# Performance work log

Measured on AMD Instinct MI355X. Metric: run time of the kernel, lower is better.

## Reference

```python
import jax, jax.numpy as jnp
import numpy as np

B, N, D = 1, 4096, 512
H, DH, M, WIN = 8, 64, 4, 512
QK_SCALE = 10.0  # qk_norm_scale


def _l2norm(t):
    # F.normalize(p=2, dim=-1) with groups=1
    n = jnp.linalg.norm(t, axis=-1, keepdims=True)
    return t / jnp.maximum(n, 1e-12)


def _rotate_half(t):
    t1, t2 = jnp.split(t, 2, axis=-1)
    return jnp.concatenate([-t2, t1], axis=-1)


def setup_inputs() -> dict:
    key = jax.random.key(0)
    ks = jax.random.split(key, 9)
    s = 0.02
    x = jax.random.normal(ks[0], (B, N, D), jnp.float32)
    Wq = jax.random.normal(ks[1], (D, H * DH), jnp.float32) * s
    Wk = jax.random.normal(ks[2], (D, H * DH), jnp.float32) * s
    Wv = jax.random.normal(ks[3], (D, H * DH), jnp.float32) * s
    Wg = jax.random.normal(ks[4], (D, H * DH), jnp.float32) * s
    bg = jnp.ones((H * DH,), jnp.float32)  # torch init: bias=1
    Wo = jax.random.normal(ks[5], (H * DH, D), jnp.float32) * s
    mem_k = jax.random.normal(ks[6], (H, M, DH), jnp.float32)
    mem_v = jax.random.normal(ks[7], (H, M, DH), jnp.float32)
    # standard rotary table, duplicated halves so rotate_half pairing matches
    half = DH // 2
    inv = 1.0 / (10000.0 ** (np.arange(half, dtype=np.float32) / half))
    f = np.outer(np.arange(N, dtype=np.float32), inv)  # [N, DH/2]
    freqs = jnp.asarray(np.concatenate([f, f], axis=-1), jnp.float32)  # [N, DH]
    return {"x": x, "Wq": Wq, "Wk": Wk, "Wv": Wv, "Wg": Wg, "bg": bg,
            "Wo": Wo, "mem_k": mem_k, "mem_v": mem_v, "freqs": freqs}


def reference(x, Wq, Wk, Wv, Wg, bg, Wo, mem_k, mem_v, freqs):
    # projections -> b h n d
    def split_heads(t):
        return t.reshape(B, N, H, DH).transpose(0, 2, 1, 3)
    q = split_heads(x @ Wq)
    k = split_heads(x @ Wk)
    v = split_heads(x @ Wv)
    # qk-norm (groups=1), scale handled via QK_SCALE later
    q = _l2norm(q)
    k = _l2norm(k)
    # rotary (l == DH so full head dim is rotated)
    cos = jnp.cos(freqs)  # [N, DH]
    sin = jnp.sin(freqs)
    q = q * cos + _rotate_half(q) * sin
    k = k * cos + _rotate_half(k) * sin
    # memory KV concat (mem_k goes through l2norm under qk_norm)
    mk = jnp.broadcast_to(_l2norm(mem_k)[None], (B, H, M, DH))
    mv = jnp.broadcast_to(mem_v[None], (B, H, M, DH))
    k = jnp.concatenate([mk, k], axis=2)  # [B,H,M+N,DH]
    v = jnp.concatenate([mv, v], axis=2)
    J = N + M
    # local window mask: queries at positions M..J-1, keys at 0..J-1
    rq = jnp.arange(M, J)
    rk = jnp.arange(J)
    dist = rq[:, None] - rk[None, :]
    allowed = (dist <= WIN) & (dist >= -WIN)  # [N, J]
    sim = jnp.einsum('bhid,bhjd->bhij', q, k) * QK_SCALE
    neg = -jnp.finfo(sim.dtype).max
    sim = jnp.where(allowed[None, None], sim, neg)
    attn = jax.nn.softmax(sim, axis=-1)
    out = jnp.einsum('bhij,bhjd->bhid', attn, v)  # [B,H,N,DH]
    out = out.transpose(0, 2, 1, 3).reshape(B, N, H * DH)
    # value gating
    gates = x @ Wg + bg
    out = out * jax.nn.sigmoid(gates)
    return out @ Wo
```

## Files before the change

### kernel.cpp

```cpp
#include <hip/hip_runtime.h>
#include <math.h>

#define TN 4096
#define DM 512
#define NH 8
#define DHD 64
#define MEM 4
#define WINR 512
#define JTOT (TN + MEM)
#define JPAD 4168
#define QK_SCALE 10.0f
#define LDA 40

typedef __attribute__((ext_vector_type(8))) short bf16x8;
typedef __attribute__((ext_vector_type(4))) float f32x4;

__device__ __forceinline__ unsigned short f2bf(float f) {
    unsigned u = __float_as_uint(f);
    u = (u + 0x7FFFu + ((u >> 16) & 1u)) >> 16;
    return (unsigned short)u;
}

__global__ __launch_bounds__(256)
void prep(const float* __restrict__ X, unsigned short* __restrict__ Xb,
          const float* __restrict__ W0, const float* __restrict__ W1,
          const float* __restrict__ W2, const float* __restrict__ W3,
          const float* __restrict__ W4, unsigned short* __restrict__ T,
          const float* __restrict__ freqs, float2* __restrict__ tab,
          const float* __restrict__ mem_k, const float* __restrict__ mem_v,
          unsigned short* __restrict__ k_b, unsigned short* __restrict__ v_b)
{
    const int b = blockIdx.x;
    const int t = threadIdx.x;

    if (b < 2048) {
        int idx = b * 256 + t;
        float4 v = *(const float4*)&X[(size_t)idx * 4];
        *(ushort4*)&Xb[(size_t)idx * 4] =
            make_ushort4(f2bf(v.x), f2bf(v.y), f2bf(v.z), f2bf(v.w));
    } else if (b < 2368) {
        __shared__ unsigned short Ts[64][68];
        int bi = b - 2048;
        int sel = bi >> 6, tile = bi & 63;
        const float* __restrict__ W =
            (sel == 0) ? W0 : (sel == 1) ? W1 : (sel == 2) ? W2 : (sel == 3) ? W3 : W4;
        unsigned short* __restrict__ Wt = T + (size_t)sel * DM * DM;
        int r0 = (tile >> 3) * 64, c0 = (tile & 7) * 64;
        #pragma unroll
        for (int p = 0; p < 4; ++p) {
            int i  = p * 16 + (t >> 4);
            int j4 = (t & 15) * 4;
            float4 v = *(const float4*)&W[(size_t)(r0 + i) * DM + c0 + j4];
            Ts[i][j4 + 0] = f2bf(v.x); Ts[i][j4 + 1] = f2bf(v.y);
            Ts[i][j4 + 2] = f2bf(v.z); Ts[i][j4 + 3] = f2bf(v.w);
        }
        __syncthreads();
        #pragma unroll
        for (int p = 0; p < 4; ++p) {
            int oc  = p * 16 + (t >> 4);
            int or4 = (t & 15) * 4;
            *(ushort4*)&Wt[(size_t)(c0 + oc) * DM + r0 + or4] =
                make_ushort4(Ts[or4 + 0][oc], Ts[or4 + 1][oc],
                             Ts[or4 + 2][oc], Ts[or4 + 3][oc]);
        }
    } else if (b < 2432) {
        int tid = (b - 2368) * 256 + t;
        #pragma unroll
        for (int e = 0; e < 16; ++e) {
            int id = e * 16384 + tid;
            float f = freqs[id];
            float sn, cs;
            sincosf(f, &sn, &cs);
            tab[id] = make_float2(cs, sn);
        }
    } else {
        int gw   = (b - 2432) * 4 + (t >> 6);
        int lane = t & 63;
        int h = gw >> 2, m = gw & 3;
        float kv = mem_k[(size_t)(h * MEM + m) * DHD + lane];
        float s = kv * kv;
        #pragma unroll
        for (int off = 1; off < 64; off <<= 1) s += __shfl_xor(s, off);
        kv = kv / fmaxf(sqrtf(s), 1e-12f);
        k_b[((size_t)h * JPAD + m) * 64 + lane] = f2bf(kv);
        v_b[((size_t)h * JPAD + m) * 64 + lane] =
            f2bf(mem_v[(size_t)(h * MEM + m) * DHD + lane]);
    }
}

__global__ __launch_bounds__(256)
void gemm_qkvg_mfma(const unsigned short* __restrict__ Xb,
                    const unsigned short* __restrict__ Wt,
                    const float2* __restrict__ tab,
                    const float* __restrict__ bg,
                    unsigned short* __restrict__ q_b,
                    unsigned short* __restrict__ k_b,
                    unsigned short* __restrict__ v_b,
                    float* __restrict__ graw)
{
    __shared__ __align__(16) unsigned short As[128][LDA];
    __shared__ __align__(16) unsigned short Bs[128][LDA];
    const int sel = blockIdx.z;
    const unsigned short* __restrict__ Wsel = Wt + (size_t)sel * DM * DM;
    const int row0 = blockIdx.x * 128;
    const int col0 = blockIdx.y * 128;
    const int t = threadIdx.x;
    const int w = t >> 6, l = t & 63;
    const int wm = w >> 1, wn = w & 1;
    const int l15 = l & 15, lh = l >> 4;

    f32x4 acc[4][4];
    #pragma unroll
    for (int mi = 0; mi < 4; ++mi)
        #pragma unroll
        for (int ni = 0; ni < 4; ++ni)
            acc[mi][ni] = (f32x4){0.f, 0.f, 0.f, 0.f};

    for (int k0 = 0; k0 < DM; k0 += 32) {
        __syncthreads();
        #pragma unroll
        for (int cc = 0; cc < 2; ++cc) {
            int c = t + cc * 256;
            int row = c >> 2, k8 = c & 3;
            *(bf16x8*)&As[row][k8 * 8] =
                *(const bf16x8*)&Xb[(size_t)(row0 + row) * DM + k0 + k8 * 8];
            *(bf16x8*)&Bs[row][k8 * 8] =
                *(const bf16x8*)&Wsel[(size_t)(col0 + row) * DM + k0 + k8 * 8];
        }
        __syncthreads();

        bf16x8 af[4], bfr[4];
        #pragma unroll
        for (int mi = 0; mi < 4; ++mi)
            af[mi] = *(const bf16x8*)&As[wm * 64 + mi * 16 + l15][lh * 8];
        #pragma unroll
        for (int ni = 0; ni < 4; ++ni)
            bfr[ni] = *(const bf16x8*)&Bs[wn * 64 + ni * 16 + l15][lh * 8];
        #pragma unroll
        for (int mi = 0; mi < 4; ++mi)
            #pragma unroll
            for (int ni = 0; ni < 4; ++ni)
                acc[mi][ni] = __builtin_amdgcn_mfma_f32_16x16x32_bf16(
                    af[mi], bfr[ni], acc[mi][ni], 0, 0, 0);
    }

    if (sel <= 1) {
        const int h = (col0 + wn * 64) >> 6;
        #pragma unroll
        for (int mi = 0; mi < 4; ++mi) {
            #pragma unroll
            for (int r = 0; r < 4; ++r) {
                float v0 = acc[mi][0][r], v1 = acc[mi][1][r];
                float v2 = acc[mi][2][r], v3 = acc[mi][3][r];
                float ss = v0 * v0 + v1 * v1 + v2 * v2 + v3 * v3;
                ss += __shfl_xor(ss, 1); ss += __shfl_xor(ss, 2);
                ss += __shfl_xor(ss, 4); ss += __shfl_xor(ss, 8);
                float inv = 1.0f / fmaxf(sqrtf(ss), 1e-12f);
                v0 *= inv; v1 *= inv; v2 *= inv; v3 *= inv;
                int n = row0 + wm * 64 + mi * 16 + lh * 4 + r;
                float2 t0 = tab[n * 64 + l15];
                float2 t1 = tab[n * 64 + 16 + l15];
                float o0 = v0 * t0.x - v2 * t0.y;
                float o1 = v1 * t1.x - v3 * t1.y;
                float o2 = v2 * t0.x + v0 * t0.y;
                float o3 = v3 * t1.x + v1 * t1.y;
                unsigned short* dst = (sel == 0)
                    ? &q_b[((size_t)h * TN + n) * 64]
                    : &k_b[((size_t)h * JPAD + MEM + n) * 64];
                dst[l15]      = f2bf(o0);
                dst[16 + l15] = f2bf(o1);
                dst[32 + l15] = f2bf(o2);
                dst[48 + l15] = f2bf(o3);
            }
        }
    } else if (sel == 2) {
        const int h = (col0 + wn * 64) >> 6;
        #pragma unroll
        for (int mi = 0; mi < 4; ++mi)
            #pragma unroll
            for (int ni = 0; ni < 4; ++ni) {
                int d = ni * 16 + l15;
                #pragma unroll
                for (int r = 0; r < 4; ++r) {
                    int grow = row0 + wm * 64 + mi * 16 + lh * 4 + r;
                    v_b[((size_t)h * JPAD + MEM + grow) * 64 + d] = f2bf(acc[mi][ni][r]);
                }
            }
    } else {
        #pragma unroll
        for (int mi = 0; mi < 4; ++mi)
            #pragma unroll
            for (int ni = 0; ni < 4; ++ni) {
                int gcol = col0 + wn * 64 + ni * 16 + l15;
                float bgv = bg[gcol];
                #pragma unroll
                for (int r = 0; r < 4; ++r) {
                    int grow = row0 + wm * 64 + mi * 16 + lh * 4 + r;
                    float g = acc[mi][ni][r] + bgv;
                    graw[(size_t)grow * DM + gcol] = 1.0f / (1.0f + __expf(-g));
                }
            }
    }
}

__global__ __launch_bounds__(256)
void gemm_out_mfma(const unsigned short* __restrict__ Ab,
                   const unsigned short* __restrict__ Wot,
                   float* __restrict__ C)
{
    __shared__ __align__(16) unsigned short As[128][LDA];
    __shared__ __align__(16) unsigned short Bs[128][LDA];
    const int row0 = blockIdx.x * 128;
    const int col0 = blockIdx.y * 128;
    const int t = threadIdx.x;
    const int w = t >> 6, l = t & 63;
    const int wm = w >> 1, wn = w & 1;

    f32x4 acc[4][4];
    #pragma unroll
    for (int mi = 0; mi < 4; ++mi)
        #pragma unroll
        for (int ni = 0; ni < 4; ++ni)
            acc[mi][ni] = (f32x4){0.f, 0.f, 0.f, 0.f};

    for (int k0 = 0; k0 < DM; k0 += 32) {
        __syncthreads();
        #pragma unroll
        for (int cc = 0; cc < 2; ++cc) {
            int c = t + cc * 256;
            int row = c >> 2, k8 = c & 3;
            *(bf16x8*)&As[row][k8 * 8] =
                *(const bf16x8*)&Ab[(size_t)(row0 + row) * DM + k0 + k8 * 8];
            *(bf16x8*)&Bs[row][k8 * 8] =
                *(const bf16x8*)&Wot[(size_t)(col0 + row) * DM + k0 + k8 * 8];
        }
        __syncthreads();

        bf16x8 af[4], bfr[4];
        #pragma unroll
        for (int mi = 0; mi < 4; ++mi)
            af[mi] = *(const bf16x8*)&As[wm * 64 + mi * 16 + (l & 15)][(l >> 4) * 8];
        #pragma unroll
        for (int ni = 0; ni < 4; ++ni)
            bfr[ni] = *(const bf16x8*)&Bs[wn * 64 + ni * 16 + (l & 15)][(l >> 4) * 8];
        #pragma unroll
        for (int mi = 0; mi < 4; ++mi)
            #pragma unroll
            for (int ni = 0; ni < 4; ++ni)
                acc[mi][ni] = __builtin_amdgcn_mfma_f32_16x16x32_bf16(
                    af[mi], bfr[ni], acc[mi][ni], 0, 0, 0);
    }

    #pragma unroll
    for (int mi = 0; mi < 4; ++mi)
        #pragma unroll
        for (int ni = 0; ni < 4; ++ni) {
            int gcol = col0 + wn * 64 + ni * 16 + (l & 15);
            #pragma unroll
            for (int r = 0; r < 4; ++r) {
                int grow = row0 + wm * 64 + mi * 16 + (l >> 4) * 4 + r;
                C[(size_t)grow * DM + gcol] = acc[mi][ni][r];
            }
        }
}

__global__ __launch_bounds__(256)
void attn_mfma(const unsigned short* __restrict__ qb,
               const unsigned short* __restrict__ kb,
               const unsigned short* __restrict__ vb,
               const float* __restrict__ gate,
               unsigned short* __restrict__ attnb)
{
    __shared__ __align__(16) unsigned short Qs[64][72];
    __shared__ __align__(16) unsigned short Ks[64][72];
    __shared__ __align__(16) unsigned short Vt[64][72];
    __shared__ __align__(16) unsigned short Ps[64][72];

    const int sw   = (blockIdx.x & 7) * 64 + (blockIdx.x >> 3);
    const int head = sw >> 6;
    const int n0   = (sw & 63) * 64;
    const int t = threadIdx.x;
    const int wid = t >> 6;
    const int l = t & 63;
    const int l15 = l & 15, lh = l >> 4;

    #pragma unroll
    for (int it = 0; it < 2; ++it) {
        int idx = t + it * 256;
        int row = idx >> 3, c8 = (idx & 7) * 8;
        *(bf16x8*)&Qs[row][c8] =
            *(const bf16x8*)&qb[((size_t)(head * TN + n0 + row)) * 64 + c8];
    }

    f32x4 oacc[4];
    #pragma unroll
    for (int dt = 0; dt < 4; ++dt) oacc[dt] = (f32x4){0.f, 0.f, 0.f, 0.f};
    float lpart[4] = {0.f, 0.f, 0.f, 0.f};

    const int p_base = MEM + n0;
    const int kstart = max(0, p_base - WINR);
    const int kend   = min(JTOT, p_base + 63 + WINR + 1);

    const int srow = t >> 3, sc8 = (t & 7) * 8;
    const int srow2 = (t + 256) >> 3, sc82 = ((t + 256) & 7) * 8;
    const int vj = t & 63, vd0 = (t >> 6) * 8;
    const int vj2 = (t + 256) & 63, vd02 = ((t + 256) >> 6) * 8;
    bf16x8 kr0, kr1, vr0, vr1;

    kr0 = *(const bf16x8*)&kb[((size_t)head * JPAD + kstart + srow) * 64 + sc8];
    kr1 = *(const bf16x8*)&kb[((size_t)head * JPAD + kstart + srow2) * 64 + sc82];
    vr0 = *(const bf16x8*)&vb[((size_t)head * JPAD + kstart + vj) * 64 + vd0];
    vr1 = *(const bf16x8*)&vb[((size_t)head * JPAD + kstart + vj2) * 64 + vd02];

    for (int j0 = kstart; j0 < kend; j0 += 64) {
        __syncthreads();
        *(bf16x8*)&Ks[srow][sc8]   = kr0;
        *(bf16x8*)&Ks[srow2][sc82] = kr1;
        #pragma unroll
        for (int i = 0; i < 8; ++i) Vt[vd0 + i][vj]   = (unsigned short)vr0[i];
        #pragma unroll
        for (int i = 0; i < 8; ++i) Vt[vd02 + i][vj2] = (unsigned short)vr1[i];
        __syncthreads();

        if (j0 + 64 < kend) {
            int jn = j0 + 64;
            kr0 = *(const bf16x8*)&kb[((size_t)head * JPAD + jn + srow) * 64 + sc8];
            kr1 = *(const bf16x8*)&kb[((size_t)head * JPAD + jn + srow2) * 64 + sc82];
            vr0 = *(const bf16x8*)&vb[((size_t)head * JPAD + jn + vj) * 64 + vd0];
            vr1 = *(const bf16x8*)&vb[((size_t)head * JPAD + jn + vj2) * 64 + vd02];
        }

        f32x4 sacc[4];
        #pragma unroll
        for (int kt = 0; kt < 4; ++kt) sacc[kt] = (f32x4){0.f, 0.f, 0.f, 0.f};
        __builtin_amdgcn_s_setprio(1);
        #pragma unroll
        for (int s = 0; s < 2; ++s) {
            bf16x8 a = *(const bf16x8*)&Qs[wid * 16 + l15][s * 32 + lh * 8];
            #pragma unroll
            for (int kt = 0; kt < 4; ++kt) {
                bf16x8 b = *(const bf16x8*)&Ks[kt * 16 + l15][s * 32 + lh * 8];
                sacc[kt] = __builtin_amdgcn_mfma_f32_16x16x32_bf16(a, b, sacc[kt], 0, 0, 0);
            }
        }
        __builtin_amdgcn_s_setprio(0);

        #pragma unroll
        for (int r = 0; r < 4; ++r) {
            int pq = p_base + wid * 16 + lh * 4 + r;
            #pragma unroll
            for (int kt = 0; kt < 4; ++kt) {
                int j = j0 + kt * 16 + l15;
                int dist = pq - j;
                bool ok = (dist <= WINR) && (dist >= -WINR) && (j < JTOT);
                float pe = ok ? __expf(sacc[kt][r] * QK_SCALE - 10.0f) : 0.f;
                lpart[r] += pe;
                Ps[wid * 16 + lh * 4 + r][kt * 16 + l15] = f2bf(pe);
            }
        }

        __builtin_amdgcn_s_setprio(1);
        #pragma unroll
        for (int s = 0; s < 2; ++s) {
            bf16x8 a = *(const bf16x8*)&Ps[wid * 16 + l15][s * 32 + lh * 8];
            #pragma unroll
            for (int dt = 0; dt < 4; ++dt) {
                bf16x8 b = *(const bf16x8*)&Vt[dt * 16 + l15][s * 32 + lh * 8];
                oacc[dt] = __builtin_amdgcn_mfma_f32_16x16x32_bf16(a, b, oacc[dt], 0, 0, 0);
            }
        }
        __builtin_amdgcn_s_setprio(0);
    }

    #pragma unroll
    for (int r = 0; r < 4; ++r) {
        float rs = lpart[r];
        rs += __shfl_xor(rs, 1); rs += __shfl_xor(rs, 2);
        rs += __shfl_xor(rs, 4); rs += __shfl_xor(rs, 8);
        float inv = 1.0f / rs;
        int n = n0 + wid * 16 + lh * 4 + r;
        #pragma unroll
        for (int dt = 0; dt < 4; ++dt) {
            int col = head * 64 + dt * 16 + l15;
            float g = gate[(size_t)n * DM + col];
            attnb[(size_t)n * DM + col] = f2bf(oacc[dt][r] * inv * g);
        }
    }
}

extern "C" void kernel_launch(void* const* d_in, const int* in_sizes, int n_in,
                              void* d_out, int out_size, void* d_ws, size_t ws_size,
                              hipStream_t stream)
{
    const float* x     = (const float*)d_in[0];
    const float* Wq    = (const float*)d_in[1];
    const float* Wk    = (const float*)d_in[2];
    const float* Wv    = (const float*)d_in[3];
    const float* Wg    = (const float*)d_in[4];
    const float* bg    = (const float*)d_in[5];
    const float* Wo    = (const float*)d_in[6];
    const float* mem_k = (const float*)d_in[7];
    const float* mem_v = (const float*)d_in[8];
    const float* freqs = (const float*)d_in[9];

    unsigned short* q_b = (unsigned short*)d_ws;
    unsigned short* k_b = q_b + (size_t)NH * TN * DHD;
    unsigned short* v_b = k_b + (size_t)NH * JPAD * DHD;
    unsigned short* Xb  = v_b + (size_t)NH * JPAD * DHD;
    unsigned short* attnb = Xb;
    unsigned short* Wt  = Xb + (size_t)TN * DM;
    float* graw = (float*)(Wt + (size_t)5 * DM * DM);
    float2* tab = (float2*)(graw + (size_t)TN * DM);

    prep<<<dim3(2440), 256, 0, stream>>>(x, Xb, Wq, Wk, Wv, Wg, Wo, Wt,
                                         freqs, tab, mem_k, mem_v, k_b, v_b);

    gemm_qkvg_mfma<<<dim3(TN / 128, DM / 128, 4), 256, 0, stream>>>(
        Xb, Wt, tab, bg, q_b, k_b, v_b, graw);

    attn_mfma<<<dim3(512), 256, 0, stream>>>(q_b, k_b, v_b, graw, attnb);

    gemm_out_mfma<<<dim3(TN / 128, DM / 128), 256, 0, stream>>>(
        attnb, Wt + (size_t)4 * DM * DM, (float*)d_out);
}
```

Measured before the change: 159.8 us.

## Split attention key tiles across two warp groups per block with final reduction

The attention kernel now launches 512 threads per block, split into two groups of four waves. Each group processes alternate 64-key tiles using its own K, V and P shared-memory buffers, and prefetches two tiles ahead. At the end, group 1 writes its partial outputs and row sums to shared memory and group 0 adds them before normalising and gating. This doubles the parallelism along the key dimension per query tile on a 512-block grid, at the cost of more shared memory, a final reduction step and possibly lower occupancy.

```diff
diff --git a/kernel.cpp b/kernel.cpp
--- a/kernel.cpp
+++ b/kernel.cpp
@@ -264,31 +264,33 @@
         }
 }
 
-__global__ __launch_bounds__(256)
+#define TILE_US (64 * 72)
+__global__ __launch_bounds__(512)
 void attn_mfma(const unsigned short* __restrict__ qb,
                const unsigned short* __restrict__ kb,
                const unsigned short* __restrict__ vb,
                const float* __restrict__ gate,
                unsigned short* __restrict__ attnb)
 {
-    __shared__ __align__(16) unsigned short Qs[64][72];
-    __shared__ __align__(16) unsigned short Ks[64][72];
-    __shared__ __align__(16) unsigned short Vt[64][72];
-    __shared__ __align__(16) unsigned short Ps[64][72];
+    __shared__ __align__(16) unsigned short smem[TILE_US * 7];
+    unsigned short* Qs = smem;
+    #define KS(g) (smem + TILE_US * (1 + (g)))
+    #define VT(g) (smem + TILE_US * (3 + (g)))
+    #define PS(g) (smem + TILE_US * (5 + (g)))
 
     const int sw   = (blockIdx.x & 7) * 64 + (blockIdx.x >> 3);
     const int head = sw >> 6;
     const int n0   = (sw & 63) * 64;
-    const int t = threadIdx.x;
-    const int wid = t >> 6;
-    const int l = t & 63;
+    const int t   = threadIdx.x;
+    const int g   = t >> 8;
+    const int tig = t & 255;
+    const int wid = (t >> 6) & 3;
+    const int l   = t & 63;
     const int l15 = l & 15, lh = l >> 4;
 
-    #pragma unroll
-    for (int it = 0; it < 2; ++it) {
-        int idx = t + it * 256;
-        int row = idx >> 3, c8 = (idx & 7) * 8;
-        *(bf16x8*)&Qs[row][c8] =
+    {
+        int row = t >> 3, c8 = (t & 7) * 8;
+        *(bf16x8*)&Qs[row * 72 + c8] =
             *(const bf16x8*)&qb[((size_t)(head * TN + n0 + row)) * 64 + c8];
     }
 
@@ -300,90 +302,125 @@
     const int p_base = MEM + n0;
     const int kstart = max(0, p_base - WINR);
     const int kend   = min(JTOT, p_base + 63 + WINR + 1);
-
-    const int srow = t >> 3, sc8 = (t & 7) * 8;
-    const int srow2 = (t + 256) >> 3, sc82 = ((t + 256) & 7) * 8;
-    const int vj = t & 63, vd0 = (t >> 6) * 8;
-    const int vj2 = (t + 256) & 63, vd02 = ((t + 256) >> 6) * 8;
+    const int ntiles = (kend - kstart + 63) >> 6;
+    const int niter  = (ntiles + 1) >> 1;
+
+    const int srow = tig >> 3, sc8 = (tig & 7) * 8;
+    const int srow2 = (tig + 256) >> 3, sc82 = ((tig + 256) & 7) * 8;
+    const int vj = tig & 63, vd0 = (tig >> 6) * 8;
+    const int vj2 = (tig + 256) & 63, vd02 = ((tig + 256) >> 6) * 8;
     bf16x8 kr0, kr1, vr0, vr1;
 
-    kr0 = *(const bf16x8*)&kb[((size_t)head * JPAD + kstart + srow) * 64 + sc8];
-    kr1 = *(const bf16x8*)&kb[((size_t)head * JPAD + kstart + srow2) * 64 + sc82];
-    vr0 = *(const bf16x8*)&vb[((size_t)head * JPAD + kstart + vj) * 64 + vd0];
-    vr1 = *(const bf16x8*)&vb[((size_t)head * JPAD + kstart + vj2) * 64 + vd02];
-
-    for (int j0 = kstart; j0 < kend; j0 += 64) {
-        __syncthreads();
-        *(bf16x8*)&Ks[srow][sc8]   = kr0;
-        *(bf16x8*)&Ks[srow2][sc82] = kr1;
-        #pragma unroll
-        for (int i = 0; i < 8; ++i) Vt[vd0 + i][vj]   = (unsigned short)vr0[i];
-        #pragma unroll
-        for (int i = 0; i < 8; ++i) Vt[vd02 + i][vj2] = (unsigned short)vr1[i];
-        __syncthreads();
-
-        if (j0 + 64 < kend) {
-            int jn = j0 + 64;
-            kr0 = *(const bf16x8*)&kb[((size_t)head * JPAD + jn + srow) * 64 + sc8];
-            kr1 = *(const bf16x8*)&kb[((size_t)head * JPAD + jn + srow2) * 64 + sc82];
-            vr0 = *(const bf16x8*)&vb[((size_t)head * JPAD + jn + vj) * 64 + vd0];
-            vr1 = *(const bf16x8*)&vb[((size_t)head * JPAD + jn + vj2) * 64 + vd02];
-        }
-
-        f32x4 sacc[4];
-        #pragma unroll
-        for (int kt = 0; kt < 4; ++kt) sacc[kt] = (f32x4){0.f, 0.f, 0.f, 0.f};
-        __builtin_amdgcn_s_setprio(1);
-        #pragma unroll
-        for (int s = 0; s < 2; ++s) {
-            bf16x8 a = *(const bf16x8*)&Qs[wid * 16 + l15][s * 32 + lh * 8];
-            #pragma unroll
-            for (int kt = 0; kt < 4; ++kt) {
-                bf16x8 b = *(const bf16x8*)&Ks[kt * 16 + l15][s * 32 + lh * 8];
-                sacc[kt] = __builtin_amdgcn_mfma_f32_16x16x32_bf16(a, b, sacc[kt], 0, 0, 0);
-            }
-        }
-        __builtin_amdgcn_s_setprio(0);
+    int tj = g;
+    {
+        int j0 = kstart + tj * 64;
+        kr0 = *(const bf16x8*)&kb[((size_t)head * JPAD + j0 + srow) * 64 + sc8];
+        kr1 = *(const bf16x8*)&kb[((size_t)head * JPAD + j0 + srow2) * 64 + sc82];
+        vr0 = *(const bf16x8*)&vb[((size_t)head * JPAD + j0 + vj) * 64 + vd0];
+        vr1 = *(const bf16x8*)&vb[((size_t)head * JPAD + j0 + vj2) * 64 + vd02];
+    }
+
+    for (int it = 0; it < niter; ++it) {
+        bool valid = (tj < ntiles);
+        __syncthreads();
+        if (valid) {
+            *(bf16x8*)&KS(g)[srow * 72 + sc8]   = kr0;
+            *(bf16x8*)&KS(g)[srow2 * 72 + sc82] = kr1;
+            #pragma unroll
+            for (int i = 0; i < 8; ++i) VT(g)[(vd0 + i) * 72 + vj]   = (unsigned short)vr0[i];
+            #pragma unroll
+            for (int i = 0; i < 8; ++i) VT(g)[(vd02 + i) * 72 + vj2] = (unsigned short)vr1[i];
+        }
+        __syncthreads();
+
+        if (valid) {
+            int j0 = kstart + tj * 64;
+            if (tj + 2 < ntiles) {
+                int jn = kstart + (tj + 2) * 64;
+                kr0 = *(const bf16x8*)&kb[((size_t)head * JPAD + jn + srow) * 64 + sc8];
+                kr1 = *(const bf16x8*)&kb[((size_t)head * JPAD + jn + srow2) * 64 + sc82];
+                vr0 = *(const bf16x8*)&vb[((size_t)head * JPAD + jn + vj) * 64 + vd0];
+                vr1 = *(const bf16x8*)&vb[((size_t)head * JPAD + jn + vj2) * 64 + vd02];
+            }
+
+            f32x4 sacc[4];
+            #pragma unroll
+            for (int kt = 0; kt < 4; ++kt) sacc[kt] = (f32x4){0.f, 0.f, 0.f, 0.f};
+            __builtin_amdgcn_s_setprio(1);
+            #pragma unroll
+            for (int s = 0; s < 2; ++s) {
+                bf16x8 a = *(const bf16x8*)&Qs[(wid * 16 + l15) * 72 + s * 32 + lh * 8];
+                #pragma unroll
+                for (int kt = 0; kt < 4; ++kt) {
+                    bf16x8 b = *(const bf16x8*)&KS(g)[(kt * 16 + l15) * 72 + s * 32 + lh * 8];
+                    sacc[kt] = __builtin_amdgcn_mfma_f32_16x16x32_bf16(a, b, sacc[kt], 0, 0, 0);
+                }
+            }
+            __builtin_amdgcn_s_setprio(0);
+
+            #pragma unroll
+            for (int r = 0; r < 4; ++r) {
+                int pq = p_base + wid * 16 + lh * 4 + r;
+                #pragma unroll
+                for (int kt = 0; kt < 4; ++kt) {
+                    int j = j0 + kt * 16 + l15;
+                    int dist = pq - j;
+                    bool ok = (dist <= WINR) && (dist >= -WINR) && (j < JTOT);
+                    float pe = ok ? __expf(sacc[kt][r] * QK_SCALE - 10.0f) : 0.f;
+                    lpart[r] += pe;
+                    PS(g)[(wid * 16 + lh * 4 + r) * 72 + kt * 16 + l15] = f2bf(pe);
+                }
+            }
+
+            __builtin_amdgcn_s_setprio(1);
+            #pragma unroll
+            for (int s = 0; s < 2; ++s) {
+                bf16x8 a = *(const bf16x8*)&PS(g)[(wid * 16 + l15) * 72 + s * 32 + lh * 8];
+                #pragma unroll
+                for (int dt = 0; dt < 4; ++dt) {
+                    bf16x8 b = *(const bf16x8*)&VT(g)[(dt * 16 + l15) * 72 + s * 32 + lh * 8];
+                    oacc[dt] = __builtin_amdgcn_mfma_f32_16x16x32_bf16(a, b, oacc[dt], 0, 0, 0);
+                }
+            }
+            __builtin_amdgcn_s_setprio(0);
+        }
+        tj += 2;
+    }
+
+    float* fbuf = (float*)smem;
+    __syncthreads();
+    if (g == 1) {
+        #pragma unroll
+        for (int dt = 0; dt < 4; ++dt)
+            #pragma unroll
+            for (int r = 0; r < 4; ++r)
+                fbuf[tig * 21 + dt * 4 + r] = oacc[dt][r];
+        #pragma unroll
+        for (int r = 0; r < 4; ++r) fbuf[tig * 21 + 16 + r] = lpart[r];
+    }
+    __syncthreads();
+    if (g == 0) {
+        #pragma unroll
+        for (int dt = 0; dt < 4; ++dt)
+            #pragma unroll
+            for (int r = 0; r < 4; ++r)
+                oacc[dt][r] += fbuf[tig * 21 + dt * 4 + r];
+        #pragma unroll
+        for (int r = 0; r < 4; ++r) lpart[r] += fbuf[tig * 21 + 16 + r];
 
         #pragma unroll
         for (int r = 0; r < 4; ++r) {
-            int pq = p_base + wid * 16 + lh * 4 + r;
-            #pragma unroll
-            for (int kt = 0; kt < 4; ++kt) {
-                int j = j0 + kt * 16 + l15;
-                int dist = pq - j;
-                bool ok = (dist <= WINR) && (dist >= -WINR) && (j < JTOT);
-                float pe = ok ? __expf(sacc[kt][r] * QK_SCALE - 10.0f) : 0.f;
-                lpart[r] += pe;
-                Ps[wid * 16 + lh * 4 + r][kt * 16 + l15] = f2bf(pe);
-            }
-        }
-
-        __builtin_amdgcn_s_setprio(1);
-        #pragma unroll
-        for (int s = 0; s < 2; ++s) {
-            bf16x8 a = *(const bf16x8*)&Ps[wid * 16 + l15][s * 32 + lh * 8];
+            float rs = lpart[r];
+            rs += __shfl_xor(rs, 1); rs += __shfl_xor(rs, 2);
+            rs += __shfl_xor(rs, 4); rs += __shfl_xor(rs, 8);
+            float inv = 1.0f / rs;
+            int n = n0 + wid * 16 + lh * 4 + r;
             #pragma unroll
             for (int dt = 0; dt < 4; ++dt) {
-                bf16x8 b = *(const bf16x8*)&Vt[dt * 16 + l15][s * 32 + lh * 8];
-                oacc[dt] = __builtin_amdgcn_mfma_f32_16x16x32_bf16(a, b, oacc[dt], 0, 0, 0);
-            }
-        }
-        __builtin_amdgcn_s_setprio(0);
-    }
-
-    #pragma unroll
-    for (int r = 0; r < 4; ++r) {
-        float rs = lpart[r];
-        rs += __shfl_xor(rs, 1); rs += __shfl_xor(rs, 2);
-        rs += __shfl_xor(rs, 4); rs += __shfl_xor(rs, 8);
-        float inv = 1.0f / rs;
-        int n = n0 + wid * 16 + lh * 4 + r;
-        #pragma unroll
-        for (int dt = 0; dt < 4; ++dt) {
-            int col = head * 64 + dt * 16 + l15;
-            float g = gate[(size_t)n * DM + col];
-            attnb[(size_t)n * DM + col] = f2bf(oacc[dt][r] * inv * g);
+                int col = head * 64 + dt * 16 + l15;
+                float gv = gate[(size_t)n * DM + col];
+                attnb[(size_t)n * DM + col] = f2bf(oacc[dt][r] * inv * gv);
+            }
         }
     }
 }
@@ -418,7 +455,7 @@
     gemm_qkvg_mfma<<<dim3(TN / 128, DM / 128, 4), 256, 0, stream>>>(
         Xb, Wt, tab, bg, q_b, k_b, v_b, graw);
 
-    attn_mfma<<<dim3(512), 256, 0, stream>>>(q_b, k_b, v_b, graw, attnb);
+    attn_mfma<<<dim3(512), 512, 0, stream>>>(q_b, k_b, v_b, graw, attnb);
 
     gemm_out_mfma<<<dim3(TN / 128, DM / 128), 256, 0, stream>>>(
         attnb, Wt + (size_t)4 * DM * DM, (float*)d_out);
```

New measurement: 157.0 us. No clear change (-1.8%).
